# Kernel optimization log

Hardware: AMD Instinct MI355X
Metric: run time of the kernel (lower is better)

Reference implementation:

```python
import jax, jax.numpy as jnp
import numpy as np

N = 4_000_000

def setup_inputs() -> dict:
    key = jax.random.key(0)
    k1, k2 = jax.random.split(key)
    quaternions = jax.random.normal(k1, (N, 4), dtype=jnp.float32)
    scales = jax.random.uniform(k2, (N, 3), dtype=jnp.float32)
    return {"quaternions": quaternions, "scales": scales}

def _build_rotation(q):
    # q: [N,4] already normalized, (r, x, y, z) convention as in 3DGS build_rotation
    r, x, y, z = q[:, 0], q[:, 1], q[:, 2], q[:, 3]
    R = jnp.stack([
        1 - 2 * (y * y + z * z), 2 * (x * y - r * z),     2 * (x * z + r * y),
        2 * (x * y + r * z),     1 - 2 * (x * x + z * z), 2 * (y * z - r * x),
        2 * (x * z - r * y),     2 * (y * z + r * x),     1 - 2 * (x * x + y * y),
    ], axis=-1)  # [N,9]
    return R.reshape(-1, 3, 3)

def reference(quaternions, scales):
    # F.normalize(p=2, dim=1) with eps clamp
    norm = jnp.maximum(jnp.linalg.norm(quaternions, axis=1, keepdims=True), 1e-12)
    q = quaternions / norm
    R = _build_rotation(q)                      # [N,3,3]
    M = R * scales[:, None, :]                  # R @ diag(scales), [N,3,3]
    covariance = jnp.einsum('nij,nkj->nik', M, M)  # M @ M^T
    return covariance
```

## Files before the change

### kernel.cpp

```cpp
#include <hip/hip_runtime.h>
#include <hip/hip_bf16.h>


#define BLK 256

__device__ __forceinline__ void compute_cov(float4 q, float sx, float sy, float sz,
                                            float* c )
{
    float r = q.x, x = q.y, y = q.z, z = q.w;
    float nrm = sqrtf(r*r + x*x + y*y + z*z);
    nrm = fmaxf(nrm, 1e-12f);
    float inv = 1.0f / nrm;
    r *= inv; x *= inv; y *= inv; z *= inv;

    float R00 = 1.0f - 2.0f*(y*y + z*z);
    float R01 = 2.0f*(x*y - r*z);
    float R02 = 2.0f*(x*z + r*y);
    float R10 = 2.0f*(x*y + r*z);
    float R11 = 1.0f - 2.0f*(x*x + z*z);
    float R12 = 2.0f*(y*z - r*x);
    float R20 = 2.0f*(x*z - r*y);
    float R21 = 2.0f*(y*z + r*x);
    float R22 = 1.0f - 2.0f*(x*x + y*y);

    float sx2 = sx*sx, sy2 = sy*sy, sz2 = sz*sz;

    c[0] = R00*R00*sx2 + R01*R01*sy2 + R02*R02*sz2;
    c[1] = R00*R10*sx2 + R01*R11*sy2 + R02*R12*sz2;
    c[2] = R00*R20*sx2 + R01*R21*sy2 + R02*R22*sz2;
    c[3] = R10*R10*sx2 + R11*R11*sy2 + R12*R12*sz2;
    c[4] = R10*R20*sx2 + R11*R21*sy2 + R12*R22*sz2;
    c[5] = R20*R20*sx2 + R21*R21*sy2 + R22*R22*sz2;
}

__global__ __launch_bounds__(BLK) void gaussians_cov_kernel(
    const float4* __restrict__ quat,
    const float*  __restrict__ scales,
    float*        __restrict__ out,
    int n)
{
    __shared__ float s_sc[BLK * 3];
    __shared__ float s_cov[BLK * 9];

    const int t = threadIdx.x;
    const long long base = (long long)blockIdx.x * BLK;

    if (base + BLK <= n) {
        if (t < (BLK * 3) / 4) {
            ((float4*)s_sc)[t] =
                ((const float4*)scales)[(long long)blockIdx.x * ((BLK * 3) / 4) + t];
        }
        float4 q = quat[base + t];
        __syncthreads();

        float sx = s_sc[3*t], sy = s_sc[3*t+1], sz = s_sc[3*t+2];

        float c[6];
        compute_cov(q, sx, sy, sz, c);

        float* cp = s_cov + 9 * t;
        cp[0] = c[0]; cp[1] = c[1]; cp[2] = c[2];
        cp[3] = c[1]; cp[4] = c[3]; cp[5] = c[4];
        cp[6] = c[2]; cp[7] = c[4]; cp[8] = c[5];
        __syncthreads();

        const float4* src = (const float4*)s_cov;
        float4* dst = (float4*)(out + base * 9);
        #pragma unroll
        for (int k = 0; k < (BLK * 9) / 4; k += BLK) {
            int idx = k + t;
            if (idx < (BLK * 9) / 4) dst[idx] = src[idx];
        }
    } else {
        long long i = base + t;
        if (i < n) {
            float4 q = quat[i];
            const float* sp = scales + 3 * i;
            float c[6];
            compute_cov(q, sp[0], sp[1], sp[2], c);
            float* op = out + 9 * i;
            op[0] = c[0]; op[1] = c[1]; op[2] = c[2];
            op[3] = c[1]; op[4] = c[3]; op[5] = c[4];
            op[6] = c[2]; op[7] = c[4]; op[8] = c[5];
        }
    }
}

extern "C" void kernel_launch(void* const* d_in, const int* in_sizes, int n_in,
                              void* d_out, int out_size, void* d_ws, size_t ws_size,
                              hipStream_t stream)
{
    const float4* quat   = (const float4*)d_in[0];
    const float*  scales = (const float*)d_in[1];
    float*        out    = (float*)d_out;
    int n = in_sizes[0] / 4;

    int grid = (n + BLK - 1) / BLK;
    gaussians_cov_kernel<<<grid, BLK, 0, stream>>>(quat, scales, out, n);
}
```

Baseline: 225.4 us.

## Process two gaussians per thread with nontemporal loads/stores and direct scale loads

```diff
diff --git a/kernel.cpp b/kernel.cpp
--- a/kernel.cpp
+++ b/kernel.cpp
@@ -3,8 +3,12 @@
 
 
 #define BLK 256
+#define PPT 2
+#define PPB (BLK * PPT)
 
-__device__ __forceinline__ void compute_cov(float4 q, float sx, float sy, float sz,
+typedef float vfloat4 __attribute__((ext_vector_type(4)));
+
+__device__ __forceinline__ void compute_cov(vfloat4 q, float sx, float sy, float sz,
                                             float* c )
 {
     float r = q.x, x = q.y, y = q.z, z = q.w;
@@ -34,54 +38,60 @@
 }
 
 __global__ __launch_bounds__(BLK) void gaussians_cov_kernel(
-    const float4* __restrict__ quat,
-    const float*  __restrict__ scales,
-    float*        __restrict__ out,
+    const vfloat4* __restrict__ quat,
+    const float*   __restrict__ scales,
+    float*         __restrict__ out,
     int n)
 {
-    __shared__ float s_sc[BLK * 3];
-    __shared__ float s_cov[BLK * 9];
+    __shared__ float s_cov[PPB * 9];
 
     const int t = threadIdx.x;
-    const long long base = (long long)blockIdx.x * BLK;
+    const long long base = (long long)blockIdx.x * PPB;
 
-    if (base + BLK <= n) {
-        if (t < (BLK * 3) / 4) {
-            ((float4*)s_sc)[t] =
-                ((const float4*)scales)[(long long)blockIdx.x * ((BLK * 3) / 4) + t];
-        }
-        float4 q = quat[base + t];
+    if (base + PPB <= n) {
+        vfloat4 q0 = __builtin_nontemporal_load(&quat[base + t]);
+        vfloat4 q1 = __builtin_nontemporal_load(&quat[base + BLK + t]);
+
+        const float* sp0 = scales + 3 * (base + t);
+        const float* sp1 = scales + 3 * (base + BLK + t);
+        float s0x = sp0[0], s0y = sp0[1], s0z = sp0[2];
+        float s1x = sp1[0], s1y = sp1[1], s1z = sp1[2];
+
+        float c0[6], c1[6];
+        compute_cov(q0, s0x, s0y, s0z, c0);
+        compute_cov(q1, s1x, s1y, s1z, c1);
+
+        float* cp0 = s_cov + 9 * t;
+        cp0[0] = c0[0]; cp0[1] = c0[1]; cp0[2] = c0[2];
+        cp0[3] = c0[1]; cp0[4] = c0[3]; cp0[5] = c0[4];
+        cp0[6] = c0[2]; cp0[7] = c0[4]; cp0[8] = c0[5];
+        float* cp1 = s_cov + 9 * (BLK + t);
+        cp1[0] = c1[0]; cp1[1] = c1[1]; cp1[2] = c1[2];
+        cp1[3] = c1[1]; cp1[4] = c1[3]; cp1[5] = c1[4];
+        cp1[6] = c1[2]; cp1[7] = c1[4]; cp1[8] = c1[5];
         __syncthreads();
 
-        float sx = s_sc[3*t], sy = s_sc[3*t+1], sz = s_sc[3*t+2];
-
-        float c[6];
-        compute_cov(q, sx, sy, sz, c);
-
-        float* cp = s_cov + 9 * t;
-        cp[0] = c[0]; cp[1] = c[1]; cp[2] = c[2];
-        cp[3] = c[1]; cp[4] = c[3]; cp[5] = c[4];
-        cp[6] = c[2]; cp[7] = c[4]; cp[8] = c[5];
-        __syncthreads();
-
-        const float4* src = (const float4*)s_cov;
-        float4* dst = (float4*)(out + base * 9);
+        const vfloat4* src = (const vfloat4*)s_cov;
+        vfloat4* dst = (vfloat4*)(out + base * 9);
         #pragma unroll
-        for (int k = 0; k < (BLK * 9) / 4; k += BLK) {
-            int idx = k + t;
-            if (idx < (BLK * 9) / 4) dst[idx] = src[idx];
+        for (int k = 0; k < 5; ++k) {
+            int idx = k * BLK + t;
+            if (idx < (PPB * 9) / 4)
+                __builtin_nontemporal_store(src[idx], &dst[idx]);
         }
     } else {
-        long long i = base + t;
-        if (i < n) {
-            float4 q = quat[i];
-            const float* sp = scales + 3 * i;
-            float c[6];
-            compute_cov(q, sp[0], sp[1], sp[2], c);
-            float* op = out + 9 * i;
-            op[0] = c[0]; op[1] = c[1]; op[2] = c[2];
-            op[3] = c[1]; op[4] = c[3]; op[5] = c[4];
-            op[6] = c[2]; op[7] = c[4]; op[8] = c[5];
+        for (int p = 0; p < PPT; ++p) {
+            long long i = base + p * BLK + t;
+            if (i < n) {
+                vfloat4 q = quat[i];
+                const float* sp = scales + 3 * i;
+                float c[6];
+                compute_cov(q, sp[0], sp[1], sp[2], c);
+                float* op = out + 9 * i;
+                op[0] = c[0]; op[1] = c[1]; op[2] = c[2];
+                op[3] = c[1]; op[4] = c[3]; op[5] = c[4];
+                op[6] = c[2]; op[7] = c[4]; op[8] = c[5];
+            }
         }
     }
 }
@@ -90,11 +100,11 @@
                               void* d_out, int out_size, void* d_ws, size_t ws_size,
                               hipStream_t stream)
 {
-    const float4* quat   = (const float4*)d_in[0];
-    const float*  scales = (const float*)d_in[1];
-    float*        out    = (float*)d_out;
+    const vfloat4* quat   = (const vfloat4*)d_in[0];
+    const float*   scales = (const float*)d_in[1];
+    float*         out    = (float*)d_out;
     int n = in_sizes[0] / 4;
 
-    int grid = (n + BLK - 1) / BLK;
+    int grid = (n + PPB - 1) / PPB;
     gaussians_cov_kernel<<<grid, BLK, 0, stream>>>(quat, scales, out, n);
 }
```

Measured after the change: 221.2 us. No clear change (-1.9%).
